# Kernel tuning notes

Measured on AMD Instinct MI355X. Metric: run time of the kernel, lower is better.

## Reference

```python
import jax, jax.numpy as jnp
import numpy as np

# dims
B, L, T, D = 8, 27, 256, 1152
GS = 3            # group_size
G = L // GS       # num_groups = 9
DD = 512          # downsample_dim
H, HD = 8, 64     # heads, head_dim
NQ = 1            # num_queries
OD = 2048         # output_dim
SCALE = 1.0 / float(np.sqrt(HD))


def setup_inputs() -> dict:
    key = jax.random.key(0)
    ks = jax.random.split(key, 12)
    s = 0.02
    return {
        "K": jax.random.normal(ks[0], (B, L, T, D), jnp.float32),
        "V": jax.random.normal(ks[1], (B, L, T, D), jnp.float32),
        # learnable queries: one (NQ, D) per layer, stacked -> (L, NQ, D)
        "query": jax.random.normal(ks[2], (L, NQ, D), jnp.float32),
        # per-group linear params (flax Linear: y = x @ W + b, W is (in, out))
        "Wq": jax.random.normal(ks[3], (G, D, DD), jnp.float32) * s,
        "bq": jnp.zeros((G, DD), jnp.float32),
        "Wk": jax.random.normal(ks[4], (G, D, DD), jnp.float32) * s,
        "bk": jnp.zeros((G, DD), jnp.float32),
        "Wv": jax.random.normal(ks[5], (G, D, DD), jnp.float32) * s,
        "bv": jnp.zeros((G, DD), jnp.float32),
        "Wo": jax.random.normal(ks[6], (G, DD, OD), jnp.float32) * s,
        "bo": jnp.zeros((G, OD), jnp.float32),
    }


def reference(K, V, query, Wq, bq, Wk, bk, Wv, bv, Wo, bo):
    # group the L layer axis: (B, G, GS, T, D); layers in a group share weights
    Kg = K.reshape(B, G, GS, T, D)
    Vg = V.reshape(B, G, GS, T, D)
    qg = query.reshape(G, GS, NQ, D)

    # projections (batched over groups; replaces L tiny per-layer linears)
    Qp = jnp.einsum('gsnd,gdf->gsnf', qg, Wq) + bq[:, None, None, :]
    Qp = Qp.reshape(G, GS, NQ, H, HD)
    Kp = (jnp.einsum('bgstd,gdf->bgstf', Kg, Wk)
          + bk[None, :, None, None, :]).reshape(B, G, GS, T, H, HD)
    Vp = (jnp.einsum('bgstd,gdf->bgstf', Vg, Wv)
          + bv[None, :, None, None, :]).reshape(B, G, GS, T, H, HD)

    # cross-attention: learnable query attends over T tokens per layer
    scores = jnp.einsum('gsnhe,bgsthe->bgsnht', Qp, Kp) * SCALE
    attn = jax.nn.softmax(scores, axis=-1)
    pooled = jnp.einsum('bgsnht,bgsthe->bgsnhe', attn, Vp)
    pooled = pooled.mean(axis=3)  # mean over queries (== squeeze when NQ=1) -> (B,G,GS,H,HD)

    # original does pooled.transpose(0,2,1).reshape(B, DD): head_dim-major flatten
    pooled = pooled.transpose(0, 1, 2, 4, 3).reshape(B, G, GS, DD)

    out = jnp.einsum('bgsf,gfo->bgso', pooled, Wo) + bo[None, :, None, :]
    return out.reshape(B, L, OD)
```

## Files before the change

### kernel.cpp

```cpp
#include <hip/hip_runtime.h>
#include <stdint.h>


__global__ __launch_bounds__(256) void qproj(
    const float* __restrict__ query, const float* __restrict__ Wq,
    const float* __restrict__ bq, float* __restrict__ Qp)
{
  const int l = blockIdx.x, g = l / 3;
  const int fb = blockIdx.y * 64;
  __shared__ float q[1152];
  __shared__ float part[4][64];
  for (int i = threadIdx.x; i < 1152; i += 256) q[i] = query[(size_t)l * 1152 + i];
  __syncthreads();
  const int fi = threadIdx.x & 63;
  const int kq = threadIdx.x >> 6;
  const float* W = Wq + (size_t)g * 1152 * 512 + fb + fi;
  float a0 = 0.f, a1 = 0.f;
  const int d0 = kq * 288;
#pragma unroll 4
  for (int d = d0; d < d0 + 288; d += 2) {
    a0 += q[d]     * W[(size_t)d * 512];
    a1 += q[d + 1] * W[(size_t)(d + 1) * 512];
  }
  part[kq][fi] = a0 + a1;
  __syncthreads();
  if (threadIdx.x < 64) {
    const int f = fb + threadIdx.x;
    float r = part[0][threadIdx.x] + part[1][threadIdx.x]
            + part[2][threadIdx.x] + part[3][threadIdx.x];
    Qp[l * 512 + f] = (r + bq[g * 512 + f]) * 0.125f;
  }
}

__global__ __launch_bounds__(256) void qk_mat(
    const float* __restrict__ Qp, const float* __restrict__ Wk,
    float* __restrict__ Qk)
{
  const int gidx = blockIdx.x * 256 + threadIdx.x;
  const int eg   = gidx & 3;
  const int item = gidx >> 2;
  const int l    = item / 9216;
  const int rem  = item % 9216;
  const int h    = rem / 1152;
  const int d    = rem % 1152;
  const int g    = l / 3;
  const float4* q4 = (const float4*)(Qp + l * 512 + h * 64 + eg * 16);
  const float4* w4 = (const float4*)(Wk + (size_t)g * 1152 * 512 + (size_t)d * 512 + h * 64 + eg * 16);
  float acc = 0.f;
#pragma unroll
  for (int e = 0; e < 4; e++) {
    const float4 a = q4[e], b = w4[e];
    acc += a.x * b.x + a.y * b.y + a.z * b.z + a.w * b.w;
  }
  acc += __shfl_xor(acc, 1, 64);
  acc += __shfl_xor(acc, 2, 64);
  if (eg == 0) Qk[((size_t)l * 1152 + d) * 8 + h] = acc;
}

__global__ __launch_bounds__(256) void score_k(
    const float* __restrict__ K, const float* __restrict__ Qk,
    float* __restrict__ scores)
{
  const int bl = blockIdx.x;
  const int tq = blockIdx.y;
  const int l = bl % 27;
  const int tid = threadIdx.x;
  const int tt = tid & 63;
  const int ds = tid >> 6;

  __shared__ float lds[64 * 195];

  const float* Kbase = K + ((size_t)bl * 256 + tq * 64) * 1152;
  const float* qkl = Qk + (size_t)l * 1152 * 8;

  float sc[8] = {0.f, 0.f, 0.f, 0.f, 0.f, 0.f, 0.f, 0.f};

  for (int dc = 0; dc < 6; dc++) {
    __syncthreads();
#pragma unroll
    for (int it = 0; it < 12; it++) {
      const int flat = it * 256 + tid;
      const int row = flat / 48, col = flat % 48;
      const float4 v = *(const float4*)(Kbase + (size_t)row * 1152 + dc * 192 + col * 4);
      float* p = &lds[row * 195 + col * 4];
      p[0] = v.x; p[1] = v.y; p[2] = v.z; p[3] = v.w;
    }
    __syncthreads();
    const float* q0 = qkl + (size_t)(dc * 192 + ds * 48) * 8;
    const float* krow = &lds[tt * 195 + ds * 48];
#pragma unroll 6
    for (int j = 0; j < 48; j++) {
      const float kv = krow[j];
      const float* q = q0 + j * 8;
#pragma unroll
      for (int h = 0; h < 8; h++) sc[h] = fmaf(kv, q[h], sc[h]);
    }
  }

  __syncthreads();
#pragma unroll
  for (int h = 0; h < 8; h++) lds[(ds * 64 + tt) * 8 + h] = sc[h];
  __syncthreads();
  if (tid < 64) {
    float* dst = scores + ((size_t)bl * 256 + tq * 64 + tid) * 8;
#pragma unroll
    for (int h = 0; h < 8; h++)
      dst[h] = (lds[(0 * 64 + tid) * 8 + h] + lds[(1 * 64 + tid) * 8 + h])
             + (lds[(2 * 64 + tid) * 8 + h] + lds[(3 * 64 + tid) * 8 + h]);
  }
}

__global__ __launch_bounds__(256) void softmax_k(
    const float* __restrict__ scores, float* __restrict__ attn)
{
  const int bl = blockIdx.x;
  const int t = threadIdx.x;
  const int wid = t >> 6, lane = t & 63;
  __shared__ float red[4][8], red2[4][8];

  float sc[8];
  const float* src = scores + ((size_t)bl * 256 + t) * 8;
#pragma unroll
  for (int h = 0; h < 8; h++) sc[h] = src[h];
#pragma unroll
  for (int h = 0; h < 8; h++) {
    float m = sc[h];
#pragma unroll
    for (int o = 1; o < 64; o <<= 1) m = fmaxf(m, __shfl_xor(m, o, 64));
    if (lane == 0) red[wid][h] = m;
  }
  __syncthreads();
  float p[8];
#pragma unroll
  for (int h = 0; h < 8; h++) {
    const float M = fmaxf(fmaxf(red[0][h], red[1][h]), fmaxf(red[2][h], red[3][h]));
    p[h] = __expf(sc[h] - M);
    float s = p[h];
#pragma unroll
    for (int o = 1; o < 64; o <<= 1) s += __shfl_xor(s, o, 64);
    if (lane == 0) red2[wid][h] = s;
  }
  __syncthreads();
  float* dst = attn + ((size_t)bl * 256 + t) * 8;
#pragma unroll
  for (int h = 0; h < 8; h++) {
    const float S = red2[0][h] + red2[1][h] + red2[2][h] + red2[3][h];
    dst[h] = p[h] * (1.0f / S);
  }
}

__global__ __launch_bounds__(384) void va_k(
    const float* __restrict__ V, const float* __restrict__ attn,
    float* __restrict__ VA)
{
  const int bl = blockIdx.x;
  const int dt = blockIdx.y;
  const int d  = dt * 384 + threadIdx.x;

  const float* Vbase = V + (size_t)bl * 256 * 1152 + d;
  const float* ab = attn + (size_t)bl * 256 * 8;

  float acc[8] = {0.f, 0.f, 0.f, 0.f, 0.f, 0.f, 0.f, 0.f};
#pragma unroll 4
  for (int t = 0; t < 256; t++) {
    const float v = Vbase[(size_t)t * 1152];
    const float* av = ab + t * 8;
#pragma unroll
    for (int h = 0; h < 8; h++) acc[h] = fmaf(av[h], v, acc[h]);
  }
  float* dst = VA + (size_t)bl * 8 * 1152 + d;
#pragma unroll
  for (int h = 0; h < 8; h++) dst[(size_t)h * 1152] = acc[h];
}

__global__ __launch_bounds__(512) void pv_mat(
    const float* __restrict__ VA, const float* __restrict__ Wv,
    float* __restrict__ psum)
{
  const int l = blockIdx.x, g = l / 3, h = blockIdx.y, dz = blockIdx.z;
  const int b = threadIdx.x >> 6, lane = threadIdx.x & 63;
  const int bl = b * 27 + l;
  const float* W = Wv + (size_t)g * 1152 * 512 + h * 64 + lane;
  const float* va = VA + ((size_t)bl * 8 + h) * 1152;
  const int d0 = dz * 288;
  float a0 = 0.f, a1 = 0.f, a2 = 0.f, a3 = 0.f;
#pragma unroll 2
  for (int d = d0; d < d0 + 288; d += 4) {
    a0 = fmaf(va[d],     W[(size_t)(d)     * 512], a0);
    a1 = fmaf(va[d + 1], W[(size_t)(d + 1) * 512], a1);
    a2 = fmaf(va[d + 2], W[(size_t)(d + 2) * 512], a2);
    a3 = fmaf(va[d + 3], W[(size_t)(d + 3) * 512], a3);
  }
  psum[((size_t)dz * 216 + bl) * 512 + lane * 8 + h] = (a0 + a1) + (a2 + a3);
}

__global__ __launch_bounds__(256) void out_gemm(
    const float* __restrict__ psum, const float* __restrict__ bv,
    const float* __restrict__ Wo, const float* __restrict__ bo,
    float* __restrict__ out)
{
  const int l = blockIdx.x, g = l / 3;
  const int n = blockIdx.y * 256 + threadIdx.x;
  __shared__ float pl[8][512];
  for (int i = threadIdx.x; i < 4096; i += 256) {
    const int b = i >> 9, f = i & 511;
    const int bl = b * 27 + l;
    const int e = f >> 3, h = f & 7;
    float v = bv[g * 512 + h * 64 + e];
#pragma unroll
    for (int dz = 0; dz < 4; dz++)
      v += psum[((size_t)dz * 216 + bl) * 512 + f];
    pl[b][f] = v;
  }
  __syncthreads();
  const float* W = Wo + (size_t)g * 512 * 2048 + n;
  float acc[8] = {0.f, 0.f, 0.f, 0.f, 0.f, 0.f, 0.f, 0.f};
#pragma unroll 4
  for (int f = 0; f < 512; f++) {
    const float w = W[(size_t)f * 2048];
#pragma unroll
    for (int b = 0; b < 8; b++) acc[b] += pl[b][f] * w;
  }
  const float bb = bo[g * 2048 + n];
#pragma unroll
  for (int b = 0; b < 8; b++)
    out[(size_t)(b * 27 + l) * 2048 + n] = acc[b] + bb;
}

__global__ __launch_bounds__(256) void zfill(float* __restrict__ out, int n) {
  const int i = blockIdx.x * 256 + threadIdx.x;
  if (i < n) out[i] = 0.f;
}

extern "C" void kernel_launch(void* const* d_in, const int* in_sizes, int n_in,
                              void* d_out, int out_size, void* d_ws, size_t ws_size,
                              hipStream_t stream)
{
  float* out = (float*)d_out;

  bool ok = (n_in == 11) && (out_size == 8 * 27 * 2048);
  if (ok) {
    const int expect[11] = {
      8 * 27 * 256 * 1152,
      8 * 27 * 256 * 1152,
      27 * 1 * 1152,
      9 * 1152 * 512,
      9 * 512,
      9 * 1152 * 512,
      9 * 512,
      9 * 1152 * 512,
      9 * 512,
      9 * 512 * 2048,
      9 * 2048
    };
    for (int i = 0; i < 11; i++) ok = ok && (in_sizes[i] == expect[i]);
  }
  const size_t NEED = 14321664;
  ok = ok && (ws_size >= NEED);

  if (!ok) {
    zfill<<<dim3((out_size + 255) / 256), dim3(256), 0, stream>>>(out, out_size);
    return;
  }

  const float* Kin   = (const float*)d_in[0];
  const float* Vin   = (const float*)d_in[1];
  const float* query = (const float*)d_in[2];
  const float* Wq    = (const float*)d_in[3];
  const float* bq    = (const float*)d_in[4];
  const float* Wk    = (const float*)d_in[5];
  const float* Wv    = (const float*)d_in[7];
  const float* bvp   = (const float*)d_in[8];
  const float* Wo    = (const float*)d_in[9];
  const float* bo    = (const float*)d_in[10];

  char* ws = (char*)d_ws;
  float* Qpw     = (float*)(ws);
  float* Qkw     = (float*)(ws + 55296);
  float* scoresw = (float*)(ws + 1050624);
  float* attnw   = (float*)(ws + 2820096);
  float* VAw     = (float*)(ws + 4589568);
  float* psumw   = (float*)(ws + 12552192);

  qproj    <<<dim3(27, 8),    dim3(256), 0, stream>>>(query, Wq, bq, Qpw);
  qk_mat   <<<dim3(3888),     dim3(256), 0, stream>>>(Qpw, Wk, Qkw);
  score_k  <<<dim3(216, 4),   dim3(256), 0, stream>>>(Kin, Qkw, scoresw);
  softmax_k<<<dim3(216),      dim3(256), 0, stream>>>(scoresw, attnw);
  va_k     <<<dim3(216, 3),   dim3(384), 0, stream>>>(Vin, attnw, VAw);
  pv_mat   <<<dim3(27, 8, 4), dim3(512), 0, stream>>>(VAw, Wv, psumw);
  out_gemm <<<dim3(27, 8),    dim3(256), 0, stream>>>(psumw, bvp, Wo, bo, out);
}
```

Before: 320.9 us.

## Register-tile score kernel over tokens and d-slices with Qk staged in LDS

Reworks the score kernel's thread mapping so each thread owns 4 tokens by a 12-wide d-slice, 16 d-groups in total, instead of 1 token by a 48-wide slice. Qk chunks are staged in shared memory and held in registers, so each loaded Q value is reused across 4 tokens instead of being read from global memory for every token. K rows are padded to 196 floats and written and read with float4 accesses. The cost is higher register pressure, from 32 accumulators plus 96 q values, and a larger 16-way reduction through LDS at the end.

```diff
diff --git a/kernel.cpp b/kernel.cpp
--- a/kernel.cpp
+++ b/kernel.cpp
@@ -65,15 +65,20 @@
   const int tq = blockIdx.y;
   const int l = bl % 27;
   const int tid = threadIdx.x;
-  const int tt = tid & 63;
-  const int ds = tid >> 6;
-
-  __shared__ float lds[64 * 195];
+  const int tg = tid & 15;
+  const int dg = tid >> 4;
+
+  __shared__ __align__(16) float Kt[64 * 196];
+  __shared__ __align__(16) float Qs[192 * 8];
 
   const float* Kbase = K + ((size_t)bl * 256 + tq * 64) * 1152;
-  const float* qkl = Qk + (size_t)l * 1152 * 8;
-
-  float sc[8] = {0.f, 0.f, 0.f, 0.f, 0.f, 0.f, 0.f, 0.f};
+  const float* Qbase = Qk + (size_t)l * 1152 * 8;
+
+  float acc[4][8];
+#pragma unroll
+  for (int tt = 0; tt < 4; tt++)
+#pragma unroll
+    for (int h = 0; h < 8; h++) acc[tt][h] = 0.f;
 
   for (int dc = 0; dc < 6; dc++) {
     __syncthreads();
@@ -82,31 +87,49 @@
       const int flat = it * 256 + tid;
       const int row = flat / 48, col = flat % 48;
       const float4 v = *(const float4*)(Kbase + (size_t)row * 1152 + dc * 192 + col * 4);
-      float* p = &lds[row * 195 + col * 4];
-      p[0] = v.x; p[1] = v.y; p[2] = v.z; p[3] = v.w;
+      *(float4*)&Kt[row * 196 + col * 4] = v;
+    }
+    {
+      const float4* qsrc = (const float4*)(Qbase + (size_t)dc * 192 * 8);
+      *(float4*)&Qs[tid * 4] = qsrc[tid];
+      if (tid < 128) *(float4*)&Qs[(256 + tid) * 4] = qsrc[256 + tid];
     }
     __syncthreads();
-    const float* q0 = qkl + (size_t)(dc * 192 + ds * 48) * 8;
-    const float* krow = &lds[tt * 195 + ds * 48];
-#pragma unroll 6
-    for (int j = 0; j < 48; j++) {
-      const float kv = krow[j];
-      const float* q = q0 + j * 8;
-#pragma unroll
-      for (int h = 0; h < 8; h++) sc[h] = fmaf(kv, q[h], sc[h]);
+
+    float q[12][8];
+#pragma unroll
+    for (int j = 0; j < 12; j++) {
+      *(float4*)&q[j][0] = *(const float4*)&Qs[(dg * 12 + j) * 8];
+      *(float4*)&q[j][4] = *(const float4*)&Qs[(dg * 12 + j) * 8 + 4];
     }
-  }
-
-  __syncthreads();
-#pragma unroll
-  for (int h = 0; h < 8; h++) lds[(ds * 64 + tt) * 8 + h] = sc[h];
-  __syncthreads();
-  if (tid < 64) {
-    float* dst = scores + ((size_t)bl * 256 + tq * 64 + tid) * 8;
-#pragma unroll
-    for (int h = 0; h < 8; h++)
-      dst[h] = (lds[(0 * 64 + tid) * 8 + h] + lds[(1 * 64 + tid) * 8 + h])
-             + (lds[(2 * 64 + tid) * 8 + h] + lds[(3 * 64 + tid) * 8 + h]);
+#pragma unroll
+    for (int tt = 0; tt < 4; tt++) {
+      float kv[12];
+      const float* kr = &Kt[(tg * 4 + tt) * 196 + dg * 12];
+      *(float4*)&kv[0] = *(const float4*)(kr + 0);
+      *(float4*)&kv[4] = *(const float4*)(kr + 4);
+      *(float4*)&kv[8] = *(const float4*)(kr + 8);
+#pragma unroll
+      for (int j = 0; j < 12; j++)
+#pragma unroll
+        for (int h = 0; h < 8; h++)
+          acc[tt][h] = fmaf(kv[j], q[j][h], acc[tt][h]);
+    }
+  }
+
+  __syncthreads();
+#pragma unroll
+  for (int tt = 0; tt < 4; tt++) {
+    *(float4*)&Kt[(dg * 64 + tg * 4 + tt) * 8    ] = *(float4*)&acc[tt][0];
+    *(float4*)&Kt[(dg * 64 + tg * 4 + tt) * 8 + 4] = *(float4*)&acc[tt][4];
+  }
+  __syncthreads();
+  for (int out = tid; out < 512; out += 256) {
+    const int t = out >> 3, h = out & 7;
+    float s = 0.f;
+#pragma unroll
+    for (int dgi = 0; dgi < 16; dgi++) s += Kt[(dgi * 64 + t) * 8 + h];
+    scores[((size_t)bl * 256 + tq * 64 + t) * 8 + h] = s;
   }
 }
 
```

After: 279.5 us. 12.9% less time.
